# Performance work log

Measured on AMD Instinct MI355X. Metric: run time of the kernel, lower is better.

Reference implementation:

```python
import jax, jax.numpy as jnp
import numpy as np

OUT_SIZE = 7
SPATIAL_SCALE = 0.125
SAMPLE_NUM = 2


def setup_inputs() -> dict:
    key = jax.random.key(0)
    kf, kb, kc, kwh, ka = jax.random.split(key, 5)
    B, C, H, W = 2, 256, 128, 128
    N = 1024
    features = jax.random.normal(kf, (B, C, H, W), dtype=jnp.float32)
    # rois: (batch_idx, cx, cy, w, h, angle) in IMAGE coordinates (stride-8 map -> 1024px image)
    batch_idx = jax.random.randint(kb, (N,), 0, B).astype(jnp.float32)
    ctr = jax.random.uniform(kc, (N, 2), dtype=jnp.float32) * (jnp.array([W, H], jnp.float32) / SPATIAL_SCALE)
    wh = jax.random.uniform(kwh, (N, 2), dtype=jnp.float32, minval=8.0, maxval=256.0)
    ang = jax.random.uniform(ka, (N, 1), dtype=jnp.float32, minval=-np.pi, maxval=np.pi)
    rois = jnp.concatenate([batch_idx[:, None], ctr, wh, ang], axis=1)
    return {"features": features, "rois": rois}


def roi_align_rotated(features, rois, out_size, spatial_scale, sample_num):
    """Faithful port of the AerialDetection/mmcv RoIAlignRotated CUDA forward."""
    B, C, H, W = features.shape
    P, S = out_size, sample_num
    b = rois[:, 0].astype(jnp.int32)                       # [N]
    cx = rois[:, 1] * spatial_scale
    cy = rois[:, 2] * spatial_scale
    rw = jnp.maximum(rois[:, 3] * spatial_scale, 1.0)
    rh = jnp.maximum(rois[:, 4] * spatial_scale, 1.0)
    theta = rois[:, 5]
    bin_h = rh / P
    bin_w = rw / P
    # sample-point offsets in the roi-centered (unrotated) frame: [N, P, S]
    pidx = jnp.arange(P, dtype=jnp.float32)
    sub = (jnp.arange(S, dtype=jnp.float32) + 0.5) / S
    grid = pidx[None, :, None] + sub[None, None, :]        # [1, P, S]
    yy = -0.5 * rh[:, None, None] + grid * bin_h[:, None, None]   # [N, P, S]
    xx = -0.5 * rw[:, None, None] + grid * bin_w[:, None, None]   # [N, P, S]
    cos_t = jnp.cos(theta)[:, None, None, None, None]
    sin_t = jnp.sin(theta)[:, None, None, None, None]
    yy5 = yy[:, :, None, :, None]                          # [N, P(h), 1, S(iy), 1]
    xx5 = xx[:, None, :, None, :]                          # [N, 1, P(w), 1, S(ix)]
    # rotate into feature-map coordinates: [N, P, P, S, S]
    x = xx5 * cos_t - yy5 * sin_t + cx[:, None, None, None, None]
    y = xx5 * sin_t + yy5 * cos_t + cy[:, None, None, None, None]
    valid = (y > -1.0) & (y < H) & (x > -1.0) & (x < W)
    y = jnp.clip(y, 0.0, H - 1)
    x = jnp.clip(x, 0.0, W - 1)
    y0 = jnp.floor(y).astype(jnp.int32)
    x0 = jnp.floor(x).astype(jnp.int32)
    y1 = jnp.minimum(y0 + 1, H - 1)
    x1 = jnp.minimum(x0 + 1, W - 1)
    ly = y - y0.astype(y.dtype)
    lx = x - x0.astype(x.dtype)
    hy, hx = 1.0 - ly, 1.0 - lx
    bb = b[:, None, None, None, None]

    def gather(yi, xi):
        # advanced indexing -> [N, P, P, S, S, C]
        return features[bb, :, yi, xi]

    val = (gather(y0, x0) * (hy * hx)[..., None]
           + gather(y0, x1) * (hy * lx)[..., None]
           + gather(y1, x0) * (ly * hx)[..., None]
           + gather(y1, x1) * (ly * lx)[..., None])
    val = jnp.where(valid[..., None], val, 0.0)
    out = val.sum(axis=(3, 4)) / (S * S)                   # [N, P, P, C]
    return jnp.transpose(out, (0, 3, 1, 2))                # [N, C, P, P]


def reference(features, rois):
    return roi_align_rotated(features, rois, OUT_SIZE, SPATIAL_SCALE, SAMPLE_NUM)
```

## Files before the change

### kernel.cpp

```cpp
#include <hip/hip_runtime.h>
#include <hip/hip_fp16.h>

constexpr int Bc = 2, Cc = 256, Hc = 128, Wc = 128;
constexpr int POUT = 7;
constexpr int SNUM = 2;
constexpr float SCALE = 0.125f;
constexpr int PP = POUT * POUT;
constexpr int QBINS = 13;
constexpr int SPITCH = 260;

__global__ __launch_bounds__(256) void transpose_nchw_nhwc_h(
    const float* __restrict__ in, __half* __restrict__ out) {
  __shared__ __half tile[64][66];
  const int HW = Hc * Wc;
  const int b = blockIdx.z;
  const int c0 = blockIdx.y * 64;
  const int hw0 = blockIdx.x * 64;
  const int tid = threadIdx.x;
  const int tx = tid & 63, ty = tid >> 6;
#pragma unroll
  for (int j = ty; j < 64; j += 4)
    tile[j][tx] = __float2half(in[(size_t)(b * Cc + c0 + j) * HW + hw0 + tx]);
  __syncthreads();
  const int wtx = tid & 31;
  const int wrow = tid >> 5;
#pragma unroll
  for (int j = wrow; j < 64; j += 8) {
    __half2 h2;
    h2.x = tile[2 * wtx][j];
    h2.y = tile[2 * wtx + 1][j];
    *(__half2*)&out[(size_t)(b * HW + hw0 + j) * Cc + c0 + 2 * wtx] = h2;
  }
}

constexpr int NBUCK = 32;
__global__ __launch_bounds__(1024) void order_rois_kernel(
    const float* __restrict__ rois, int* __restrict__ order, int N) {
  __shared__ int cnt[NBUCK];
  __shared__ int base_[NBUCK];
  __shared__ unsigned char mykey[1024];
  const int t = threadIdx.x;
  if (t < NBUCK) cnt[t] = 0;
  __syncthreads();
  if (t < N) {
    const float* r = rois + (size_t)t * 6;
    const int bb = (int)r[0];
    int cy = (int)(r[2] * SCALE);
    cy = min(max(cy, 0), Hc - 1);
    const int bk = ((bb & 1) << 4) | (cy >> 3);
    mykey[t] = (unsigned char)bk;
    atomicAdd(&cnt[bk], 1);
  }
  __syncthreads();
  if (t == 0) {
    int s = 0;
#pragma unroll
    for (int i = 0; i < NBUCK; ++i) { base_[i] = s; s += cnt[i]; }
  }
  __syncthreads();
  if (t < N) {
    const int pos = atomicAdd(&base_[mykey[t]], 1);
    order[pos] = t;
  }
}

template <int GG>
__device__ __forceinline__ void writeout(const float* stage, float* out,
                                         size_t outbase, int tid) {
  int cc = tid / GG;
  int g = tid - cc * GG;
  constexpr int STEP_CC = 256 / GG;
  constexpr int STEP_G = 256 % GG;
#pragma unroll 4
  for (int it = 0; it < GG; ++it) {
    out[outbase + (size_t)cc * PP + g] = stage[g * SPITCH + cc];
    g += STEP_G;
    cc += STEP_CC;
    if (g >= GG) { g -= GG; cc += 1; }
  }
}

__global__ __launch_bounds__(256) void roi_align_q_kernel(
    const __half* __restrict__ feat, const float* __restrict__ rois,
    const int* __restrict__ order, float* __restrict__ out, int N) {
  __shared__ int s_off[QBINS * 8];
  __shared__ int s_w[QBINS * 16];
  __shared__ float stage[QBINS * SPITCH];

  const int b = blockIdx.x;
  int n, q;
  if (order) {
    const int M = N >> 3;
    const int j = b >> 3;
    n = order[(b & 7) * M + (j >> 2)];
    q = j & 3;
  } else {
    n = b % N;
    q = b / N;
  }
  const int pp0 = q * QBINS;
  const int G = min(QBINS, PP - pp0);

  const int tid = threadIdx.x;
  const int w = tid >> 6;
  const int lane = tid & 63;
  const int run_s = (w * G) >> 2;
  const int run_e = ((w + 1) * G) >> 2;

  const int nb = run_e - run_s;
  if (lane < 4 * nb) {
    const int slot = run_s + (lane >> 2), s = lane & 3;
    const int iy = s >> 1, ix = s & 1;
    const int bin = pp0 + slot;
    const float* r = rois + (size_t)n * 6;
    const int ph = bin / POUT, pw = bin - (bin / POUT) * POUT;
    const int bb = (int)r[0];
    const float cx = r[1] * SCALE, cy = r[2] * SCALE;
    const float rw = fmaxf(r[3] * SCALE, 1.0f);
    const float rh = fmaxf(r[4] * SCALE, 1.0f);
    float sn, cs;
    __sincosf(r[5], &sn, &cs);
    const float bh = rh * (1.0f / POUT), bw = rw * (1.0f / POUT);

    const float yy = -0.5f * rh + ((float)ph + (iy + 0.5f) * (1.0f / SNUM)) * bh;
    const float xx = -0.5f * rw + ((float)pw + (ix + 0.5f) * (1.0f / SNUM)) * bw;
    float x = xx * cs - yy * sn + cx;
    float y = xx * sn + yy * cs + cy;
    const bool valid =
        (y > -1.0f) && (y < (float)Hc) && (x > -1.0f) && (x < (float)Wc);
    y = fminf(fmaxf(y, 0.0f), (float)(Hc - 1));
    x = fminf(fmaxf(x, 0.0f), (float)(Wc - 1));
    const int y0 = (int)floorf(y), x0 = (int)floorf(x);
    const int y1 = min(y0 + 1, Hc - 1);
    const float ly = y - (float)y0, lx = x - (float)x0;
    const float hy = 1.0f - ly, hx = 1.0f - lx;
    const float vs = valid ? (1.0f / (SNUM * SNUM)) : 0.0f;

    s_off[slot * 8 + s * 2 + 0] = ((bb * Hc + y0) * Wc + x0) * Cc;
    s_off[slot * 8 + s * 2 + 1] = ((bb * Hc + y1) * Wc + x0) * Cc;

    const float wts[4] = {hy * hx * vs, hy * lx * vs, ly * hx * vs,
                          ly * lx * vs};
#pragma unroll
    for (int k = 0; k < 4; ++k) {
      union { __half2 h; int i; } u;
      u.h = __float2half2_rn(wts[k]);
      s_w[slot * 16 + s * 4 + k] = u.i;
    }
  }

  const int e16 = lane << 3;
  const int hsel = (lane >> 5) & 1;
  const int ch0 = (lane & 31) << 3;

  for (int g = run_s; g < run_e; ++g) {
    int rbase[8];
#pragma unroll
    for (int k = 0; k < 8; ++k)
      rbase[k] = __builtin_amdgcn_readfirstlane(s_off[g * 8 + k]);

    int wsel[8];
#pragma unroll
    for (int s = 0; s < 4; ++s) {
      wsel[2 * s + 0] = s_w[g * 16 + s * 4 + hsel];
      wsel[2 * s + 1] = s_w[g * 16 + s * 4 + 2 + hsel];
    }

    uint4 v[8];
#pragma unroll
    for (int k = 0; k < 8; ++k)
      v[k] = *(const uint4*)(feat + rbase[k] + e16);

    __half2 acc[4];
#pragma unroll
    for (int i = 0; i < 4; ++i) acc[i] = __float2half2_rn(0.f);
#pragma unroll
    for (int k = 0; k < 8; ++k) {
      union { int i; __half2 h; } uw;
      uw.i = wsel[k];
      const __half2* pv = reinterpret_cast<const __half2*>(&v[k]);
#pragma unroll
      for (int i = 0; i < 4; ++i) acc[i] = __hfma2(uw.h, pv[i], acc[i]);
    }

#pragma unroll
    for (int i = 0; i < 4; ++i) {
      int ai = *reinterpret_cast<int*>(&acc[i]);
      int oi = __shfl_xor(ai, 32, 64);
      acc[i] = __hadd2(acc[i], *reinterpret_cast<__half2*>(&oi));
    }

    const float2 f0 = __half22float2(acc[0]);
    const float2 f1 = __half22float2(acc[1]);
    const float2 f2 = __half22float2(acc[2]);
    const float2 f3 = __half22float2(acc[3]);
    float* sp = &stage[g * SPITCH + ch0];
    if (lane < 32)
      *(float4*)sp = make_float4(f0.x, f0.y, f1.x, f1.y);
    else
      *(float4*)(sp + 4) = make_float4(f2.x, f2.y, f3.x, f3.y);
  }
  __syncthreads();

  const size_t outbase = (size_t)n * (Cc * PP) + pp0;
  if (G == QBINS)
    writeout<QBINS>(stage, out, outbase, tid);
  else
    writeout<PP - 3 * QBINS>(stage, out, outbase, tid);
}

__global__ __launch_bounds__(256) void roi_align_nchw_kernel(
    const float* __restrict__ feat, const float* __restrict__ rois,
    float* __restrict__ out) {
  __shared__ int s_off[PP * 16];
  __shared__ float s_w[PP * 16];
  const int n = blockIdx.x;
  const int tid = threadIdx.x;
  if (tid < PP) {
    const float* r = rois + (size_t)n * 6;
    const int ph = tid / POUT, pw = tid % POUT;
    const int b = (int)r[0];
    const float cx = r[1] * SCALE, cy = r[2] * SCALE;
    const float rw = fmaxf(r[3] * SCALE, 1.0f);
    const float rh = fmaxf(r[4] * SCALE, 1.0f);
    const float theta = r[5];
    const float cs = cosf(theta), sn = sinf(theta);
    const float bh = rh * (1.0f / POUT), bw = rw * (1.0f / POUT);
#pragma unroll
    for (int iy = 0; iy < SNUM; ++iy) {
#pragma unroll
      for (int ix = 0; ix < SNUM; ++ix) {
        const float yy = -0.5f * rh + ((float)ph + (iy + 0.5f) * (1.0f / SNUM)) * bh;
        const float xx = -0.5f * rw + ((float)pw + (ix + 0.5f) * (1.0f / SNUM)) * bw;
        float x = xx * cs - yy * sn + cx;
        float y = xx * sn + yy * cs + cy;
        const bool valid =
            (y > -1.0f) && (y < (float)Hc) && (x > -1.0f) && (x < (float)Wc);
        y = fminf(fmaxf(y, 0.0f), (float)(Hc - 1));
        x = fminf(fmaxf(x, 0.0f), (float)(Wc - 1));
        const int y0 = (int)floorf(y), x0 = (int)floorf(x);
        const int y1 = min(y0 + 1, Hc - 1), x1 = min(x0 + 1, Wc - 1);
        const float ly = y - (float)y0, lx = x - (float)x0;
        const float hy = 1.0f - ly, hx = 1.0f - lx;
        const float vs = valid ? (1.0f / (SNUM * SNUM)) : 0.0f;
        const int base = tid * 16 + (iy * SNUM + ix) * 4;
        const int bb = b * Cc * Hc * Wc;
        s_off[base + 0] = bb + y0 * Wc + x0;
        s_off[base + 1] = bb + y0 * Wc + x1;
        s_off[base + 2] = bb + y1 * Wc + x0;
        s_off[base + 3] = bb + y1 * Wc + x1;
        s_w[base + 0] = hy * hx * vs;
        s_w[base + 1] = hy * lx * vs;
        s_w[base + 2] = ly * hx * vs;
        s_w[base + 3] = ly * lx * vs;
      }
    }
  }
  __syncthreads();
  const int c = tid;
  const size_t outbase = ((size_t)n * Cc + c) * PP;
  for (int pp = 0; pp < PP; ++pp) {
    float acc = 0.0f;
#pragma unroll
    for (int k = 0; k < 16; ++k) {
      acc += s_w[pp * 16 + k] *
             feat[(size_t)s_off[pp * 16 + k] + (size_t)c * (Hc * Wc)];
    }
    out[outbase + pp] = acc;
  }
}

extern "C" void kernel_launch(void* const* d_in, const int* in_sizes, int n_in,
                              void* d_out, int out_size, void* d_ws,
                              size_t ws_size, hipStream_t stream) {
  const float* features = (const float*)d_in[0];
  const float* rois = (const float*)d_in[1];
  float* out = (float*)d_out;
  const int N = in_sizes[1] / 6;

  const size_t need_h = (size_t)Bc * Cc * Hc * Wc * sizeof(__half);
  if (ws_size >= need_h + 4096) {
    __half* nhwc = (__half*)d_ws;
    dim3 tgrid((Hc * Wc) / 64, Cc / 64, Bc);
    transpose_nchw_nhwc_h<<<tgrid, 256, 0, stream>>>(features, nhwc);

    int* order = nullptr;
    const bool can_sort = (N <= 1024) && ((N & 7) == 0);
    if (can_sort) {
      order = (int*)((char*)d_ws + need_h);
      order_rois_kernel<<<1, 1024, 0, stream>>>(rois, order, N);
    }
    roi_align_q_kernel<<<4 * N, 256, 0, stream>>>(nhwc, rois, order, out, N);
  } else {
    roi_align_nchw_kernel<<<N, 256, 0, stream>>>(features, rois, out);
  }
}
```

Baseline: 42.50 us.

## Fuse ROI ordering into transpose kernel, split ROIs in halves, stage in fp16

Result: faster. 39.92 us (-6.1%).

```diff
diff --git a/kernel.cpp b/kernel.cpp
--- a/kernel.cpp
+++ b/kernel.cpp
@@ -6,12 +6,19 @@
 constexpr int SNUM = 2;
 constexpr float SCALE = 0.125f;
 constexpr int PP = POUT * POUT;
-constexpr int QBINS = 13;
-constexpr int SPITCH = 260;
+constexpr int HBINS = 25;
+constexpr int SPITCH_H = 264;
+
+constexpr int NBUCK = 32;
 
 __global__ __launch_bounds__(256) void transpose_nchw_nhwc_h(
-    const float* __restrict__ in, __half* __restrict__ out) {
+    const float* __restrict__ in, __half* __restrict__ out,
+    const float* __restrict__ rois, int* __restrict__ order, int N) {
   __shared__ __half tile[64][66];
+  __shared__ int cnt[NBUCK];
+  __shared__ int base_[NBUCK];
+  __shared__ unsigned char keys[1024];
+
   const int HW = Hc * Wc;
   const int b = blockIdx.z;
   const int c0 = blockIdx.y * 64;
@@ -31,75 +38,71 @@
     h2.y = tile[2 * wtx + 1][j];
     *(__half2*)&out[(size_t)(b * HW + hw0 + j) * Cc + c0 + 2 * wtx] = h2;
   }
-}
-
-constexpr int NBUCK = 32;
-__global__ __launch_bounds__(1024) void order_rois_kernel(
-    const float* __restrict__ rois, int* __restrict__ order, int N) {
-  __shared__ int cnt[NBUCK];
-  __shared__ int base_[NBUCK];
-  __shared__ unsigned char mykey[1024];
-  const int t = threadIdx.x;
-  if (t < NBUCK) cnt[t] = 0;
-  __syncthreads();
-  if (t < N) {
-    const float* r = rois + (size_t)t * 6;
-    const int bb = (int)r[0];
-    int cy = (int)(r[2] * SCALE);
-    cy = min(max(cy, 0), Hc - 1);
-    const int bk = ((bb & 1) << 4) | (cy >> 3);
-    mykey[t] = (unsigned char)bk;
-    atomicAdd(&cnt[bk], 1);
-  }
-  __syncthreads();
-  if (t == 0) {
-    int s = 0;
-#pragma unroll
-    for (int i = 0; i < NBUCK; ++i) { base_[i] = s; s += cnt[i]; }
-  }
-  __syncthreads();
-  if (t < N) {
-    const int pos = atomicAdd(&base_[mykey[t]], 1);
-    order[pos] = t;
+
+  const bool doSort =
+      (order != nullptr) && blockIdx.x == 0 && blockIdx.y == 0 && blockIdx.z == 0;
+  if (doSort) {
+    if (tid < NBUCK) cnt[tid] = 0;
+    __syncthreads();
+    for (int r = tid; r < N; r += 256) {
+      const float* rr = rois + (size_t)r * 6;
+      const int bb = (int)rr[0];
+      int cy = (int)(rr[2] * SCALE);
+      cy = min(max(cy, 0), Hc - 1);
+      const int bk = ((bb & 1) << 4) | (cy >> 3);
+      keys[r] = (unsigned char)bk;
+      atomicAdd(&cnt[bk], 1);
+    }
+    __syncthreads();
+    if (tid == 0) {
+      int s = 0;
+#pragma unroll
+      for (int i = 0; i < NBUCK; ++i) { base_[i] = s; s += cnt[i]; }
+    }
+    __syncthreads();
+    for (int r = tid; r < N; r += 256) {
+      const int pos = atomicAdd(&base_[keys[r]], 1);
+      order[pos] = r;
+    }
   }
 }
 
 template <int GG>
-__device__ __forceinline__ void writeout(const float* stage, float* out,
-                                         size_t outbase, int tid) {
+__device__ __forceinline__ void writeout_h(const __half* stage, float* out,
+                                           size_t outbase, int tid) {
   int cc = tid / GG;
   int g = tid - cc * GG;
   constexpr int STEP_CC = 256 / GG;
   constexpr int STEP_G = 256 % GG;
-#pragma unroll 4
+#pragma unroll 5
   for (int it = 0; it < GG; ++it) {
-    out[outbase + (size_t)cc * PP + g] = stage[g * SPITCH + cc];
+    out[outbase + (size_t)cc * PP + g] = __half2float(stage[g * SPITCH_H + cc]);
     g += STEP_G;
     cc += STEP_CC;
     if (g >= GG) { g -= GG; cc += 1; }
   }
 }
 
-__global__ __launch_bounds__(256) void roi_align_q_kernel(
+__global__ __launch_bounds__(256) void roi_align_h_kernel(
     const __half* __restrict__ feat, const float* __restrict__ rois,
     const int* __restrict__ order, float* __restrict__ out, int N) {
-  __shared__ int s_off[QBINS * 8];
-  __shared__ int s_w[QBINS * 16];
-  __shared__ float stage[QBINS * SPITCH];
+  __shared__ int s_off[HBINS * 8];
+  __shared__ int s_w[HBINS * 16];
+  __shared__ __half stage[HBINS * SPITCH_H];
 
   const int b = blockIdx.x;
-  int n, q;
+  int n, h;
   if (order) {
     const int M = N >> 3;
     const int j = b >> 3;
-    n = order[(b & 7) * M + (j >> 2)];
-    q = j & 3;
+    n = order[(b & 7) * M + (j >> 1)];
+    h = j & 1;
   } else {
     n = b % N;
-    q = b / N;
-  }
-  const int pp0 = q * QBINS;
-  const int G = min(QBINS, PP - pp0);
+    h = b / N;
+  }
+  const int pp0 = h * HBINS;
+  const int G = h == 0 ? HBINS : (PP - HBINS);
 
   const int tid = threadIdx.x;
   const int w = tid >> 6;
@@ -143,8 +146,8 @@
                           ly * lx * vs};
 #pragma unroll
     for (int k = 0; k < 4; ++k) {
-      union { __half2 h; int i; } u;
-      u.h = __float2half2_rn(wts[k]);
+      union { __half2 hh; int i; } u;
+      u.hh = __float2half2_rn(wts[k]);
       s_w[slot * 16 + s * 4 + k] = u.i;
     }
   }
@@ -176,11 +179,11 @@
     for (int i = 0; i < 4; ++i) acc[i] = __float2half2_rn(0.f);
 #pragma unroll
     for (int k = 0; k < 8; ++k) {
-      union { int i; __half2 h; } uw;
+      union { int i; __half2 hh; } uw;
       uw.i = wsel[k];
       const __half2* pv = reinterpret_cast<const __half2*>(&v[k]);
 #pragma unroll
-      for (int i = 0; i < 4; ++i) acc[i] = __hfma2(uw.h, pv[i], acc[i]);
+      for (int i = 0; i < 4; ++i) acc[i] = __hfma2(uw.hh, pv[i], acc[i]);
     }
 
 #pragma unroll
@@ -190,23 +193,20 @@
       acc[i] = __hadd2(acc[i], *reinterpret_cast<__half2*>(&oi));
     }
 
-    const float2 f0 = __half22float2(acc[0]);
-    const float2 f1 = __half22float2(acc[1]);
-    const float2 f2 = __half22float2(acc[2]);
-    const float2 f3 = __half22float2(acc[3]);
-    float* sp = &stage[g * SPITCH + ch0];
-    if (lane < 32)
-      *(float4*)sp = make_float4(f0.x, f0.y, f1.x, f1.y);
-    else
-      *(float4*)(sp + 4) = make_float4(f2.x, f2.y, f3.x, f3.y);
+    if (lane < 32) {
+      union { uint4 u; __half2 hh[4]; } pack;
+#pragma unroll
+      for (int i = 0; i < 4; ++i) pack.hh[i] = acc[i];
+      *(uint4*)&stage[g * SPITCH_H + ch0] = pack.u;
+    }
   }
   __syncthreads();
 
   const size_t outbase = (size_t)n * (Cc * PP) + pp0;
-  if (G == QBINS)
-    writeout<QBINS>(stage, out, outbase, tid);
+  if (G == HBINS)
+    writeout_h<HBINS>(stage, out, outbase, tid);
   else
-    writeout<PP - 3 * QBINS>(stage, out, outbase, tid);
+    writeout_h<PP - HBINS>(stage, out, outbase, tid);
 }
 
 __global__ __launch_bounds__(256) void roi_align_nchw_kernel(
@@ -279,18 +279,16 @@
   const int N = in_sizes[1] / 6;
 
   const size_t need_h = (size_t)Bc * Cc * Hc * Wc * sizeof(__half);
-  if (ws_size >= need_h + 4096) {
+  if (ws_size >= need_h + 8192) {
     __half* nhwc = (__half*)d_ws;
-    dim3 tgrid((Hc * Wc) / 64, Cc / 64, Bc);
-    transpose_nchw_nhwc_h<<<tgrid, 256, 0, stream>>>(features, nhwc);
-
     int* order = nullptr;
     const bool can_sort = (N <= 1024) && ((N & 7) == 0);
-    if (can_sort) {
-      order = (int*)((char*)d_ws + need_h);
-      order_rois_kernel<<<1, 1024, 0, stream>>>(rois, order, N);
-    }
-    roi_align_q_kernel<<<4 * N, 256, 0, stream>>>(nhwc, rois, order, out, N);
+    if (can_sort) order = (int*)((char*)d_ws + need_h);
+
+    dim3 tgrid((Hc * Wc) / 64, Cc / 64, Bc);
+    transpose_nchw_nhwc_h<<<tgrid, 256, 0, stream>>>(features, nhwc, rois,
+                                                     order, N);
+    roi_align_h_kernel<<<2 * N, 256, 0, stream>>>(nhwc, rois, order, out, N);
   } else {
     roi_align_nchw_kernel<<<N, 256, 0, stream>>>(features, rois, out);
   }
```
